# Kernel optimization log

Measured on AMD Instinct MI355X. Metric: run time of the kernel, lower is better.

The kernel has to match this reference:

```python
import jax, jax.numpy as jnp
import numpy as np

B, N, D = 8, 1024, 768
H = 12
HD = D // H
LN_EPS = 1e-5
EPS = 1e-8


def setup_inputs() -> dict:
    key = jax.random.key(0)
    ks = jax.random.split(key, 16)
    s = 0.02
    return {
        "x": jax.random.normal(ks[0], (B, N, D), jnp.float32),
        "low_freq_feat": jax.random.normal(ks[1], (B, N, D), jnp.float32),
        "high_freq_feat": jax.random.normal(ks[2], (B, N, D), jnp.float32),
        "W_qkv_id": jax.random.normal(ks[3], (D, 3 * D), jnp.float32) * s,
        "W_qkv_attr": jax.random.normal(ks[4], (D, 3 * D), jnp.float32) * s,
        "W_fg_id": jax.random.normal(ks[5], (D, D), jnp.float32) * s,
        "b_fg_id": jnp.zeros((D,), jnp.float32),
        "W_fg_attr": jax.random.normal(ks[6], (D, D), jnp.float32) * s,
        "b_fg_attr": jnp.zeros((D,), jnp.float32),
        "W_proj_id": jax.random.normal(ks[7], (D, D), jnp.float32) * s,
        "b_proj_id": jnp.zeros((D,), jnp.float32),
        "W_proj_attr": jax.random.normal(ks[8], (D, D), jnp.float32) * s,
        "b_proj_attr": jnp.zeros((D,), jnp.float32),
        "ln_id_g": jnp.ones((D,), jnp.float32),
        "ln_id_b": jnp.zeros((D,), jnp.float32),
        "ln_attr_g": jnp.ones((D,), jnp.float32),
        "ln_attr_b": jnp.zeros((D,), jnp.float32),
        "ortho_temperature": jnp.float32(1.0),
        "freq_guide_strength": jnp.float32(0.3),
    }


def _layernorm(x, g, b):
    mu = x.mean(-1, keepdims=True)
    var = ((x - mu) ** 2).mean(-1, keepdims=True)
    return (x - mu) * jax.lax.rsqrt(var + LN_EPS) * g + b


def reference(x, low_freq_feat, high_freq_feat,
              W_qkv_id, W_qkv_attr,
              W_fg_id, b_fg_id, W_fg_attr, b_fg_attr,
              W_proj_id, b_proj_id, W_proj_attr, b_proj_attr,
              ln_id_g, ln_id_b, ln_attr_g, ln_attr_b,
              ortho_temperature, freq_guide_strength):
    b, n, d = x.shape
    scale = HD ** -0.5

    def split_qkv(t):
        t = t.reshape(b, n, 3, H, HD).transpose(2, 0, 3, 1, 4)
        return t[0], t[1], t[2]

    q_id, k_id, v_id = split_qkv(x @ W_qkv_id)
    q_at, k_at, v_at = split_qkv(x @ W_qkv_attr)

    fs = jax.nn.sigmoid(freq_guide_strength)
    low_g = (low_freq_feat @ W_fg_id + b_fg_id).reshape(b, n, H, HD).transpose(0, 2, 1, 3)
    high_g = (high_freq_feat @ W_fg_attr + b_fg_attr).reshape(b, n, H, HD).transpose(0, 2, 1, 3)
    v_id = v_id + fs * low_g
    v_at = v_at + fs * high_g

    def soft_attn(q, k):
        a = jnp.clip(jnp.einsum('bhnd,bhmd->bhnm', q, k) * scale, -20.0, 20.0)
        return jax.nn.softmax(a, axis=-1)

    attn_id = soft_attn(q_id, k_id)
    attn_at = soft_attn(q_at, k_at)

    # soft orthogonal mask (same mask for both branches)
    overlap = ((attn_id + EPS) * (attn_at + EPS)).sum(-1, keepdims=True)
    temp = jnp.clip(ortho_temperature, 0.1, 5.0)
    mask = jax.nn.sigmoid(-overlap * temp)

    def mask_renorm(a):
        m = a * mask
        m = m / (m.sum(-1, keepdims=True) + EPS)
        return jnp.where(jnp.isnan(m), jnp.zeros_like(m), m)

    attn_id = mask_renorm(attn_id)
    attn_at = mask_renorm(attn_at)

    def branch_out(a, v, W, bias, g, beta):
        o = jnp.einsum('bhnm,bhmd->bhnd', a, v).transpose(0, 2, 1, 3).reshape(b, n, d)
        return _layernorm(o @ W + bias, g, beta)

    id_features = branch_out(attn_id, v_id, W_proj_id, b_proj_id, ln_id_g, ln_id_b)
    attr_features = branch_out(attn_at, v_at, W_proj_attr, b_proj_attr, ln_attr_g, ln_attr_b)
    return (id_features, attr_features)
```

## Files before the change

kernel.cpp:

```cpp
#include <hip/hip_runtime.h>
#include <stdint.h>


typedef __attribute__((ext_vector_type(8))) _Float16 f16x8;
typedef __attribute__((ext_vector_type(4))) _Float16 f16x4;
typedef __attribute__((ext_vector_type(4))) float    f32x4;

__device__ __forceinline__ void g2l16(const void* g, void* l) {
  __builtin_amdgcn_global_load_lds(
      (const __attribute__((address_space(1))) void*)g,
      (__attribute__((address_space(3))) void*)l, 16, 0, 0);
}

__device__ __forceinline__ void gemm128(const _Float16* __restrict__ A,
                                        const _Float16* __restrict__ Bt,
                                        int K, int m0, int n0,
                                        _Float16* As, _Float16* Bs, f32x4* acc) {
  const int tid = threadIdx.x;
  const int lane = tid & 63, w = tid >> 6;
  const int wm = (w >> 1) * 64, wn = (w & 1) * 64;
  const int l15 = lane & 15, quad = lane >> 4;
  const int srow = lane >> 2;
  const int sg = (lane & 3) ^ ((lane >> 3) & 3);
  const int scol = sg * 8;
  const int rg = (quad ^ ((l15 >> 1) & 3)) * 8;

#pragma unroll
  for (int i = 0; i < 16; i++) acc[i] = (f32x4){0.f, 0.f, 0.f, 0.f};

  const int KB = K >> 5;
#pragma unroll
  for (int i = 0; i < 2; i++) {
    int c = w * 2 + i, row = c * 16 + srow;
    g2l16(A  + (size_t)(m0 + row) * K + scol, As + c * 512);
    g2l16(Bt + (size_t)(n0 + row) * K + scol, Bs + c * 512);
  }
  for (int kb = 0; kb < KB; kb++) {
    __syncthreads();
    f16x8 a[4], b[4];
#pragma unroll
    for (int mt = 0; mt < 4; mt++)
      a[mt] = *(const f16x8*)(As + (wm + mt * 16 + l15) * 32 + rg);
#pragma unroll
    for (int nt = 0; nt < 4; nt++)
      b[nt] = *(const f16x8*)(Bs + (wn + nt * 16 + l15) * 32 + rg);
#pragma unroll
    for (int mt = 0; mt < 4; mt++)
#pragma unroll
      for (int nt = 0; nt < 4; nt++)
        acc[mt * 4 + nt] = __builtin_amdgcn_mfma_f32_16x16x32_f16(
            a[mt], b[nt], acc[mt * 4 + nt], 0, 0, 0);
    __syncthreads();
    if (kb + 1 < KB) {
      int k0 = (kb + 1) * 32;
#pragma unroll
      for (int i = 0; i < 2; i++) {
        int c = w * 2 + i, row = c * 16 + srow;
        g2l16(A  + (size_t)(m0 + row) * K + k0 + scol, As + c * 512);
        g2l16(Bt + (size_t)(n0 + row) * K + k0 + scol, Bs + c * 512);
      }
    }
  }
}

__global__ __launch_bounds__(256) void k_cast3(const float* __restrict__ s0,
                                               const float* __restrict__ s1,
                                               const float* __restrict__ s2,
                                               _Float16* __restrict__ d0,
                                               _Float16* __restrict__ d1,
                                               _Float16* __restrict__ d2) {
  int blk = blockIdx.x;
  const float* s; _Float16* d;
  if (blk < 6144)       { s = s0; d = d0; }
  else if (blk < 12288) { s = s1; d = d1; blk -= 6144; }
  else                  { s = s2; d = d2; blk -= 12288; }
  int i = blk * 256 + threadIdx.x;
  float4 v = ((const float4*)s)[i];
  f16x4 o = {(_Float16)v.x, (_Float16)v.y, (_Float16)v.z, (_Float16)v.w};
  *(f16x4*)(d + (size_t)i * 4) = o;
}

__device__ __forceinline__ void tcast32(const float* __restrict__ src,
                                        _Float16* __restrict__ dst,
                                        int N, int n0, int k0) {
  __shared__ float t[32][33];
  int tr = threadIdx.x >> 5, tc = threadIdx.x & 31;
#pragma unroll
  for (int i = 0; i < 4; i++) {
    int r = tr + i * 8;
    t[r][tc] = src[(size_t)(k0 + r) * N + n0 + tc];
  }
  __syncthreads();
#pragma unroll
  for (int i = 0; i < 4; i++) {
    int r = tr + i * 8;
    dst[(size_t)(n0 + r) * 768 + k0 + tc] = (_Float16)t[tc][r];
  }
}

__global__ __launch_bounds__(256) void k_tcast_qkv(const float* __restrict__ W0,
                                                   const float* __restrict__ W1,
                                                   _Float16* __restrict__ dst) {
  int half = blockIdx.y / 24, yy = blockIdx.y % 24;
  const float* src = half ? W1 : W0;
  _Float16* d = dst + (size_t)half * 2304 * 768;
  tcast32(src, d, 2304, blockIdx.x * 32, yy * 32);
}

__global__ __launch_bounds__(256) void k_tcast4(const float* __restrict__ W0,
                                                const float* __restrict__ W1,
                                                const float* __restrict__ W2,
                                                const float* __restrict__ W3,
                                                _Float16* __restrict__ D0,
                                                _Float16* __restrict__ D1,
                                                _Float16* __restrict__ D2,
                                                _Float16* __restrict__ D3) {
  int q = blockIdx.y / 24, yy = blockIdx.y % 24;
  const float* src; _Float16* d;
  if (q == 0)      { src = W0; d = D0; }
  else if (q == 1) { src = W1; d = D1; }
  else if (q == 2) { src = W2; d = D2; }
  else             { src = W3; d = D3; }
  tcast32(src, d, 768, blockIdx.x * 32, yy * 32);
}

__global__ __launch_bounds__(256) void k_gemm_fg2(const _Float16* __restrict__ Alo,
                                                  const _Float16* __restrict__ Ahi,
                                                  const _Float16* __restrict__ Bid,
                                                  const _Float16* __restrict__ Bat,
                                                  const float* __restrict__ bid,
                                                  const float* __restrict__ bat,
                                                  _Float16* __restrict__ LG,
                                                  _Float16* __restrict__ HG) {
  __shared__ alignas(16) _Float16 As[4096], Bs[4096];
  f32x4 acc[16];
  int half = blockIdx.x / 6;
  int n0 = (blockIdx.x % 6) * 128, m0 = blockIdx.y * 128;
  const _Float16* A = half ? Ahi : Alo;
  const _Float16* Bt = half ? Bat : Bid;
  const float* bias = half ? bat : bid;
  _Float16* out = half ? HG : LG;
  gemm128(A, Bt, 768, m0, n0, As, Bs, acc);
  int lane = threadIdx.x & 63, w = threadIdx.x >> 6;
  int wm = (w >> 1) * 64, wn = (w & 1) * 64, l15 = lane & 15, quad = lane >> 4;
#pragma unroll
  for (int mt = 0; mt < 4; mt++)
#pragma unroll
    for (int nt = 0; nt < 4; nt++) {
      int n = n0 + wn + nt * 16 + l15;
      int m = m0 + wm + mt * 16 + quad * 4;
      float bv = bias[n];
      f32x4 v = acc[mt * 4 + nt];
#pragma unroll
      for (int r = 0; r < 4; r++)
        out[(size_t)(m + r) * 768 + n] = (_Float16)(v[r] + bv);
    }
}

__global__ __launch_bounds__(256) void k_gemm_qkv(const _Float16* __restrict__ A,
                                                  const _Float16* __restrict__ Bt,
                                                  const _Float16* __restrict__ LG,
                                                  const _Float16* __restrict__ HG,
                                                  const float* __restrict__ fgs,
                                                  _Float16* __restrict__ Qb,
                                                  _Float16* __restrict__ Kb,
                                                  _Float16* __restrict__ Vtb) {
  __shared__ alignas(16) _Float16 As[4096], Bs[4096];
  f32x4 acc[16];
  int m0 = blockIdx.y * 128, n0 = blockIdx.x * 128;
  gemm128(A, Bt, 768, m0, n0, As, Bs, acc);
  int lane = threadIdx.x & 63, w = threadIdx.x >> 6;
  int wm = (w >> 1) * 64, wn = (w & 1) * 64, l15 = lane & 15, quad = lane >> 4;
  int br = n0 / 2304;
  int three = (n0 - br * 2304) / 768;
  float fs = 1.f / (1.f + __expf(-fgs[0]));
  float qscl = (three == 0) ? 0.125f * 1.44269504f : 1.0f;
  const _Float16* FG = br ? HG : LG;
#pragma unroll
  for (int mt = 0; mt < 4; mt++)
#pragma unroll
    for (int nt = 0; nt < 4; nt++) {
      int n = n0 + wn + nt * 16 + l15;
      int c = n - br * 2304 - three * 768;
      int h = c >> 6, hd = c & 63;
      int m = m0 + wm + mt * 16 + quad * 4;
      int b = m >> 10, tok = m & 1023;
      size_t head = (size_t)(br * 96 + b * 12 + h);
      f32x4 v = acc[mt * 4 + nt];
      if (three == 2) {
        f16x4 o;
#pragma unroll
        for (int r = 0; r < 4; r++)
          o[r] = (_Float16)(v[r] + fs * (float)FG[(size_t)(m + r) * 768 + c]);
        *(f16x4*)(Vtb + (head * 64 + hd) * 1024 + tok) = o;
      } else {
        _Float16* dst = (three == 0) ? Qb : Kb;
#pragma unroll
        for (int r = 0; r < 4; r++)
          dst[(head * 1024 + tok + r) * 64 + hd] = (_Float16)(v[r] * qscl);
      }
    }
}

__global__ __launch_bounds__(256, 3) void k_attn(const _Float16* __restrict__ Qb,
                                                 const _Float16* __restrict__ Kb,
                                                 const _Float16* __restrict__ Vtb,
                                                 _Float16* __restrict__ Ob) {
  __shared__ alignas(16) _Float16 Qs[128 * 64];
  __shared__ alignas(16) _Float16 Ks[128 * 64];
  __shared__ alignas(16) _Float16 Vts[64 * 128];
  int hl = blockIdx.x;
  int br = hl / 96, bh = hl % 96;
  int qbase = blockIdx.y * 128;
  const _Float16* Qh = Qb + (size_t)hl * 65536;
  const _Float16* Kh = Kb + (size_t)hl * 65536;
  const _Float16* Vth = Vtb + (size_t)hl * 65536;
  int lane = threadIdx.x & 63, w = threadIdx.x >> 6;
  int l15 = lane & 15, quad = lane >> 4;
  const int key7 = l15 & 7;

  {
    int rr = lane >> 3, sg = (lane & 7) ^ rr;
#pragma unroll
    for (int i = 0; i < 4; i++) {
      int c = w * 4 + i;
      g2l16(Qh + (size_t)(qbase + c * 8 + rr) * 64 + sg * 8, Qs + c * 512);
    }
  }
  auto stage_kv = [&](int n0) {
    int rr8 = lane >> 3, sg8 = ((lane & 7) ^ rr8) * 8;
    int rr16 = lane >> 4;
#pragma unroll
    for (int i = 0; i < 4; i++) {
      int c = w * 4 + i;
      g2l16(Kh + (size_t)(n0 + c * 8 + rr8) * 64 + sg8, Ks + c * 512);
      int vrow = c * 4 + rr16;
      int sg16 = ((lane & 15) ^ (vrow & 15)) * 8;
      g2l16(Vth + (size_t)vrow * 1024 + n0 + sg16, Vts + c * 512);
    }
  };
  stage_kv(0);

  f32x4 o[2][4];
#pragma unroll
  for (int qg = 0; qg < 2; qg++)
#pragma unroll
    for (int i = 0; i < 4; i++) o[qg][i] = (f32x4){0.f, 0.f, 0.f, 0.f};
  float rs0 = 0.f, rs1 = 0.f;
  f16x8 bq[2][2];
  const f32x4 zero = (f32x4){0.f, 0.f, 0.f, 0.f};
  const int g0 = (quad ^ key7) * 8, g1 = ((4 + quad) ^ key7) * 8;

  for (int kt = 0; kt < 8; kt++) {
    __syncthreads();
    if (kt == 0) {
#pragma unroll
      for (int qg = 0; qg < 2; qg++) {
        bq[qg][0] = *(const f16x8*)(Qs + (w * 32 + qg * 16 + l15) * 64 + g0);
        bq[qg][1] = *(const f16x8*)(Qs + (w * 32 + qg * 16 + l15) * 64 + g1);
      }
    }
    f32x4 c0, c1;
    {
      f16x8 a0 = *(const f16x8*)(Ks + l15 * 64 + g0);
      f16x8 a1 = *(const f16x8*)(Ks + l15 * 64 + g1);
      c0 = __builtin_amdgcn_mfma_f32_16x16x32_f16(a0, bq[0][0], zero, 0, 0, 0);
      c0 = __builtin_amdgcn_mfma_f32_16x16x32_f16(a1, bq[0][1], c0, 0, 0, 0);
      c1 = __builtin_amdgcn_mfma_f32_16x16x32_f16(a0, bq[1][0], zero, 0, 0, 0);
      c1 = __builtin_amdgcn_mfma_f32_16x16x32_f16(a1, bq[1][1], c1, 0, 0, 0);
    }
#pragma unroll
    for (int nt = 0; nt < 8; nt++) {
      f32x4 n0_, n1_;
      if (nt < 7) {
        f16x8 a0 = *(const f16x8*)(Ks + ((nt + 1) * 16 + l15) * 64 + g0);
        f16x8 a1 = *(const f16x8*)(Ks + ((nt + 1) * 16 + l15) * 64 + g1);
        n0_ = __builtin_amdgcn_mfma_f32_16x16x32_f16(a0, bq[0][0], zero, 0, 0, 0);
        n0_ = __builtin_amdgcn_mfma_f32_16x16x32_f16(a1, bq[0][1], n0_, 0, 0, 0);
        n1_ = __builtin_amdgcn_mfma_f32_16x16x32_f16(a0, bq[1][0], zero, 0, 0, 0);
        n1_ = __builtin_amdgcn_mfma_f32_16x16x32_f16(a1, bq[1][1], n1_, 0, 0, 0);
      }
      f16x4 pt0, pt1;
#pragma unroll
      for (int r = 0; r < 4; r++) {
        float p = __builtin_amdgcn_exp2f(c0[r]);
        rs0 += p; pt0[r] = (_Float16)p;
      }
#pragma unroll
      for (int r = 0; r < 4; r++) {
        float p = __builtin_amdgcn_exp2f(c1[r]);
        rs1 += p; pt1[r] = (_Float16)p;
      }
#pragma unroll
      for (int hdt = 0; hdt < 4; hdt++) {
        int g = ((2 * nt + (quad >> 1)) ^ l15) * 8 + (quad & 1) * 4;
        f16x4 av = *(const f16x4*)(Vts + (hdt * 16 + l15) * 128 + g);
        o[0][hdt] = __builtin_amdgcn_mfma_f32_16x16x16f16(av, pt0, o[0][hdt], 0, 0, 0);
        o[1][hdt] = __builtin_amdgcn_mfma_f32_16x16x16f16(av, pt1, o[1][hdt], 0, 0, 0);
      }
      if (nt < 7) { c0 = n0_; c1 = n1_; }
    }
    __syncthreads();
    if (kt < 7) stage_kv((kt + 1) * 128);
  }
  int b = bh / 12, h = bh % 12;
#pragma unroll
  for (int qg = 0; qg < 2; qg++) {
    float l = qg ? rs1 : rs0;
    l += __shfl_xor(l, 16);
    l += __shfl_xor(l, 32);
    float inv = 1.f / l;
    size_t rowb = ((size_t)br * 8192 + b * 1024 + qbase + w * 32 + qg * 16 + l15) * 768 +
                  h * 64;
#pragma unroll
    for (int hdt = 0; hdt < 4; hdt++) {
      f16x4 u;
#pragma unroll
      for (int r = 0; r < 4; r++) u[r] = (_Float16)(o[qg][hdt][r] * inv);
      *(f16x4*)(Ob + rowb + hdt * 16 + quad * 4) = u;
    }
  }
}

__global__ __launch_bounds__(256) void k_gemm_proj2(const _Float16* __restrict__ Aid,
                                                    const _Float16* __restrict__ Aat,
                                                    const _Float16* __restrict__ Bid,
                                                    const _Float16* __restrict__ Bat,
                                                    float* __restrict__ Yid,
                                                    float* __restrict__ Yat) {
  __shared__ alignas(16) _Float16 As[4096], Bs[4096];
  f32x4 acc[16];
  int half = blockIdx.x / 6;
  int n0 = (blockIdx.x % 6) * 128, m0 = blockIdx.y * 128;
  const _Float16* A = half ? Aat : Aid;
  const _Float16* Bt = half ? Bat : Bid;
  float* Y = half ? Yat : Yid;
  gemm128(A, Bt, 768, m0, n0, As, Bs, acc);
  int lane = threadIdx.x & 63, w = threadIdx.x >> 6;
  int wm = (w >> 1) * 64, wn = (w & 1) * 64, l15 = lane & 15, quad = lane >> 4;
#pragma unroll
  for (int mt = 0; mt < 4; mt++)
#pragma unroll
    for (int nt = 0; nt < 4; nt++) {
      int n = n0 + wn + nt * 16 + l15;
      int m = m0 + wm + mt * 16 + quad * 4;
      f32x4 v = acc[mt * 4 + nt];
#pragma unroll
      for (int r = 0; r < 4; r++) Y[(size_t)(m + r) * 768 + n] = v[r];
    }
}

__global__ __launch_bounds__(256) void k_ln(const float* __restrict__ Yid,
                                            const float* __restrict__ Yat,
                                            const float* __restrict__ bp_id,
                                            const float* __restrict__ bp_at,
                                            const float* __restrict__ g_id,
                                            const float* __restrict__ be_id,
                                            const float* __restrict__ g_at,
                                            const float* __restrict__ be_at,
                                            float* __restrict__ out) {
  int w = threadIdx.x >> 6, lane = threadIdx.x & 63;
  int r = blockIdx.x * 4 + w;
  int br = r >> 13, m = r & 8191;
  const float* Y = br ? Yat : Yid;
  const float* bp = br ? bp_at : bp_id;
  const float* g = br ? g_at : g_id;
  const float* be = br ? be_at : be_id;
  float v[12], sum = 0.f, sq = 0.f;
#pragma unroll
  for (int i = 0; i < 12; i++) {
    int c = lane + i * 64;
    float t = Y[(size_t)m * 768 + c] + bp[c];
    v[i] = t; sum += t; sq += t * t;
  }
#pragma unroll
  for (int d = 1; d < 64; d <<= 1) { sum += __shfl_xor(sum, d); sq += __shfl_xor(sq, d); }
  float mu = sum * (1.f / 768.f);
  float var = sq * (1.f / 768.f) - mu * mu;
  float rstd = rsqrtf(var + 1e-5f);
  float* op = out + (size_t)br * 6291456 + (size_t)m * 768;
#pragma unroll
  for (int i = 0; i < 12; i++) {
    int c = lane + i * 64;
    op[c] = (v[i] - mu) * rstd * g[c] + be[c];
  }
}

extern "C" void kernel_launch(void* const* d_in, const int* in_sizes, int n_in,
                              void* d_out, int out_size, void* d_ws, size_t ws_size,
                              hipStream_t stream) {
  const float* x       = (const float*)d_in[0];
  const float* lowf    = (const float*)d_in[1];
  const float* highf   = (const float*)d_in[2];
  const float* Wqkv_id = (const float*)d_in[3];
  const float* Wqkv_at = (const float*)d_in[4];
  const float* Wfg_id  = (const float*)d_in[5];
  const float* bfg_id  = (const float*)d_in[6];
  const float* Wfg_at  = (const float*)d_in[7];
  const float* bfg_at  = (const float*)d_in[8];
  const float* Wpr_id  = (const float*)d_in[9];
  const float* bpr_id  = (const float*)d_in[10];
  const float* Wpr_at  = (const float*)d_in[11];
  const float* bpr_at  = (const float*)d_in[12];
  const float* g_id    = (const float*)d_in[13];
  const float* be_id   = (const float*)d_in[14];
  const float* g_at    = (const float*)d_in[15];
  const float* be_at   = (const float*)d_in[16];
  const float* fgs     = (const float*)d_in[18];

  char* ws = (char*)d_ws;
  _Float16* x_f    = (_Float16*)(ws + 0);
  _Float16* low_f  = (_Float16*)(ws + 12582912);
  _Float16* high_f = (_Float16*)(ws + 25165824);
  _Float16* wqkvt  = (_Float16*)(ws + 37748736);
  _Float16* wfgidt = (_Float16*)(ws + 44826624);
  _Float16* wfgatt = (_Float16*)(ws + 46006272);
  _Float16* wpridt = (_Float16*)(ws + 47185920);
  _Float16* wpratt = (_Float16*)(ws + 48365568);
  _Float16* LG     = (_Float16*)(ws + 49545216);
  _Float16* HG     = (_Float16*)(ws + 62128128);
  _Float16* Qb     = (_Float16*)(ws + 74711040);
  _Float16* Kb     = (_Float16*)(ws + 99876864);
  _Float16* Vtb    = (_Float16*)(ws + 125042688);
  _Float16* Ob     = (_Float16*)(ws + 150208512);
  float* Y_id = (float*)(ws + 0);
  float* Y_at = (float*)(ws + 49545216);

  k_cast3<<<18432, 256, 0, stream>>>(x, lowf, highf, x_f, low_f, high_f);
  k_tcast_qkv<<<dim3(72, 48), 256, 0, stream>>>(Wqkv_id, Wqkv_at, wqkvt);
  k_tcast4<<<dim3(24, 96), 256, 0, stream>>>(Wfg_id, Wfg_at, Wpr_id, Wpr_at,
                                             wfgidt, wfgatt, wpridt, wpratt);
  k_gemm_fg2<<<dim3(12, 64), 256, 0, stream>>>(low_f, high_f, wfgidt, wfgatt,
                                               bfg_id, bfg_at, LG, HG);
  k_gemm_qkv<<<dim3(36, 64), 256, 0, stream>>>(x_f, wqkvt, LG, HG, fgs, Qb, Kb, Vtb);
  k_attn<<<dim3(192, 8), 256, 0, stream>>>(Qb, Kb, Vtb, Ob);
  k_gemm_proj2<<<dim3(12, 64), 256, 0, stream>>>(Ob, Ob + 6291456, wpridt, wpratt,
                                                 Y_id, Y_at);
  k_ln<<<4096, 256, 0, stream>>>(Y_id, Y_at, bpr_id, bpr_at, g_id, be_id, g_at, be_at,
                                 (float*)d_out);
}
```

Measured before the change: 425.0 us.

## Fuse freq-guide GEMM into V accumulation, swap MFMA operands for vector stores

Reorders the pipeline so the QKV GEMM writes V first and the freq-guide GEMM then adds fs*(acc+bias) straight into the transposed V buffer. This removes the LG/HG intermediate tensors and their strided reads. A templated operand swap in the MFMA lets Q/K and projection epilogues emit contiguous f16x4 stores instead of scattered scalar writes. Projection output is now stored as fp16 and the LayerNorm kernel is vectorized, halving that intermediate traffic but adding a rounding step before the bias and LayerNorm.

```diff
diff --git a/kernel.cpp b/kernel.cpp
--- a/kernel.cpp
+++ b/kernel.cpp
@@ -12,6 +12,7 @@
       (__attribute__((address_space(3))) void*)l, 16, 0, 0);
 }
 
+template <bool SWAP>
 __device__ __forceinline__ void gemm128(const _Float16* __restrict__ A,
                                         const _Float16* __restrict__ Bt,
                                         int K, int m0, int n0,
@@ -48,8 +49,9 @@
     for (int mt = 0; mt < 4; mt++)
 #pragma unroll
       for (int nt = 0; nt < 4; nt++)
-        acc[mt * 4 + nt] = __builtin_amdgcn_mfma_f32_16x16x32_f16(
-            a[mt], b[nt], acc[mt * 4 + nt], 0, 0, 0);
+        acc[mt * 4 + nt] = SWAP
+            ? __builtin_amdgcn_mfma_f32_16x16x32_f16(b[nt], a[mt], acc[mt * 4 + nt], 0, 0, 0)
+            : __builtin_amdgcn_mfma_f32_16x16x32_f16(a[mt], b[nt], acc[mt * 4 + nt], 0, 0, 0);
     __syncthreads();
     if (kb + 1 < KB) {
       int k0 = (kb + 1) * 32;
@@ -124,81 +126,97 @@
   tcast32(src, d, 768, blockIdx.x * 32, yy * 32);
 }
 
-__global__ __launch_bounds__(256) void k_gemm_fg2(const _Float16* __restrict__ Alo,
-                                                  const _Float16* __restrict__ Ahi,
-                                                  const _Float16* __restrict__ Bid,
-                                                  const _Float16* __restrict__ Bat,
-                                                  const float* __restrict__ bid,
-                                                  const float* __restrict__ bat,
-                                                  _Float16* __restrict__ LG,
-                                                  _Float16* __restrict__ HG) {
-  __shared__ alignas(16) _Float16 As[4096], Bs[4096];
-  f32x4 acc[16];
-  int half = blockIdx.x / 6;
-  int n0 = (blockIdx.x % 6) * 128, m0 = blockIdx.y * 128;
-  const _Float16* A = half ? Ahi : Alo;
-  const _Float16* Bt = half ? Bat : Bid;
-  const float* bias = half ? bat : bid;
-  _Float16* out = half ? HG : LG;
-  gemm128(A, Bt, 768, m0, n0, As, Bs, acc);
-  int lane = threadIdx.x & 63, w = threadIdx.x >> 6;
-  int wm = (w >> 1) * 64, wn = (w & 1) * 64, l15 = lane & 15, quad = lane >> 4;
-#pragma unroll
-  for (int mt = 0; mt < 4; mt++)
-#pragma unroll
-    for (int nt = 0; nt < 4; nt++) {
-      int n = n0 + wn + nt * 16 + l15;
-      int m = m0 + wm + mt * 16 + quad * 4;
-      float bv = bias[n];
-      f32x4 v = acc[mt * 4 + nt];
-#pragma unroll
-      for (int r = 0; r < 4; r++)
-        out[(size_t)(m + r) * 768 + n] = (_Float16)(v[r] + bv);
-    }
-}
-
 __global__ __launch_bounds__(256) void k_gemm_qkv(const _Float16* __restrict__ A,
                                                   const _Float16* __restrict__ Bt,
-                                                  const _Float16* __restrict__ LG,
-                                                  const _Float16* __restrict__ HG,
-                                                  const float* __restrict__ fgs,
                                                   _Float16* __restrict__ Qb,
                                                   _Float16* __restrict__ Kb,
                                                   _Float16* __restrict__ Vtb) {
   __shared__ alignas(16) _Float16 As[4096], Bs[4096];
   f32x4 acc[16];
   int m0 = blockIdx.y * 128, n0 = blockIdx.x * 128;
-  gemm128(A, Bt, 768, m0, n0, As, Bs, acc);
+  int br = n0 / 2304;
+  int three = (n0 - br * 2304) / 768;
   int lane = threadIdx.x & 63, w = threadIdx.x >> 6;
   int wm = (w >> 1) * 64, wn = (w & 1) * 64, l15 = lane & 15, quad = lane >> 4;
-  int br = n0 / 2304;
-  int three = (n0 - br * 2304) / 768;
+
+  if (three == 2) {
+    gemm128<false>(A, Bt, 768, m0, n0, As, Bs, acc);
+#pragma unroll
+    for (int mt = 0; mt < 4; mt++)
+#pragma unroll
+      for (int nt = 0; nt < 4; nt++) {
+        int n = n0 + wn + nt * 16 + l15;
+        int c = n - br * 2304 - 1536;
+        int h = c >> 6, hd = c & 63;
+        int m = m0 + wm + mt * 16 + quad * 4;
+        int b = m >> 10, tok = m & 1023;
+        size_t head = (size_t)(br * 96 + b * 12 + h);
+        f32x4 v = acc[mt * 4 + nt];
+        f16x4 o;
+#pragma unroll
+        for (int r = 0; r < 4; r++) o[r] = (_Float16)v[r];
+        *(f16x4*)(Vtb + (head * 64 + hd) * 1024 + tok) = o;
+      }
+  } else {
+    gemm128<true>(A, Bt, 768, m0, n0, As, Bs, acc);
+    float qscl = (three == 0) ? 0.125f * 1.44269504f : 1.0f;
+    _Float16* dst = (three == 0) ? Qb : Kb;
+#pragma unroll
+    for (int mt = 0; mt < 4; mt++)
+#pragma unroll
+      for (int nt = 0; nt < 4; nt++) {
+        int m = m0 + wm + mt * 16 + l15;
+        int n = n0 + wn + nt * 16 + quad * 4;
+        int c = n - br * 2304 - three * 768;
+        int h = c >> 6, hd = c & 63;
+        int b = m >> 10, tok = m & 1023;
+        size_t head = (size_t)(br * 96 + b * 12 + h);
+        f32x4 v = acc[mt * 4 + nt];
+        f16x4 o;
+#pragma unroll
+        for (int r = 0; r < 4; r++) o[r] = (_Float16)(v[r] * qscl);
+        *(f16x4*)(dst + (head * 1024 + tok) * 64 + hd) = o;
+      }
+  }
+}
+
+__global__ __launch_bounds__(256) void k_gemm_fgadd(const _Float16* __restrict__ Alo,
+                                                    const _Float16* __restrict__ Ahi,
+                                                    const _Float16* __restrict__ Bid,
+                                                    const _Float16* __restrict__ Bat,
+                                                    const float* __restrict__ bid,
+                                                    const float* __restrict__ bat,
+                                                    const float* __restrict__ fgs,
+                                                    _Float16* __restrict__ Vtb) {
+  __shared__ alignas(16) _Float16 As[4096], Bs[4096];
+  f32x4 acc[16];
+  int br = blockIdx.x / 6;
+  int n0 = (blockIdx.x % 6) * 128, m0 = blockIdx.y * 128;
+  const _Float16* A = br ? Ahi : Alo;
+  const _Float16* Bt = br ? Bat : Bid;
+  const float* bias = br ? bat : bid;
+  gemm128<false>(A, Bt, 768, m0, n0, As, Bs, acc);
   float fs = 1.f / (1.f + __expf(-fgs[0]));
-  float qscl = (three == 0) ? 0.125f * 1.44269504f : 1.0f;
-  const _Float16* FG = br ? HG : LG;
+  int lane = threadIdx.x & 63, w = threadIdx.x >> 6;
+  int wm = (w >> 1) * 64, wn = (w & 1) * 64, l15 = lane & 15, quad = lane >> 4;
 #pragma unroll
   for (int mt = 0; mt < 4; mt++)
 #pragma unroll
     for (int nt = 0; nt < 4; nt++) {
-      int n = n0 + wn + nt * 16 + l15;
-      int c = n - br * 2304 - three * 768;
+      int c = n0 + wn + nt * 16 + l15;
       int h = c >> 6, hd = c & 63;
       int m = m0 + wm + mt * 16 + quad * 4;
       int b = m >> 10, tok = m & 1023;
       size_t head = (size_t)(br * 96 + b * 12 + h);
+      float bv = bias[c];
       f32x4 v = acc[mt * 4 + nt];
-      if (three == 2) {
-        f16x4 o;
-#pragma unroll
-        for (int r = 0; r < 4; r++)
-          o[r] = (_Float16)(v[r] + fs * (float)FG[(size_t)(m + r) * 768 + c]);
-        *(f16x4*)(Vtb + (head * 64 + hd) * 1024 + tok) = o;
-      } else {
-        _Float16* dst = (three == 0) ? Qb : Kb;
-#pragma unroll
-        for (int r = 0; r < 4; r++)
-          dst[(head * 1024 + tok + r) * 64 + hd] = (_Float16)(v[r] * qscl);
-      }
+      _Float16* p = Vtb + (head * 64 + hd) * 1024 + tok;
+      f16x4 old = *(const f16x4*)p;
+      f16x4 o;
+#pragma unroll
+      for (int r = 0; r < 4; r++)
+        o[r] = (_Float16)((float)old[r] + fs * (v[r] + bv));
+      *(f16x4*)p = o;
     }
 }
 
@@ -326,32 +344,34 @@
                                                     const _Float16* __restrict__ Aat,
                                                     const _Float16* __restrict__ Bid,
                                                     const _Float16* __restrict__ Bat,
-                                                    float* __restrict__ Yid,
-                                                    float* __restrict__ Yat) {
+                                                    _Float16* __restrict__ Yid,
+                                                    _Float16* __restrict__ Yat) {
   __shared__ alignas(16) _Float16 As[4096], Bs[4096];
   f32x4 acc[16];
   int half = blockIdx.x / 6;
   int n0 = (blockIdx.x % 6) * 128, m0 = blockIdx.y * 128;
   const _Float16* A = half ? Aat : Aid;
   const _Float16* Bt = half ? Bat : Bid;
-  float* Y = half ? Yat : Yid;
-  gemm128(A, Bt, 768, m0, n0, As, Bs, acc);
+  _Float16* Y = half ? Yat : Yid;
+  gemm128<true>(A, Bt, 768, m0, n0, As, Bs, acc);
   int lane = threadIdx.x & 63, w = threadIdx.x >> 6;
   int wm = (w >> 1) * 64, wn = (w & 1) * 64, l15 = lane & 15, quad = lane >> 4;
 #pragma unroll
   for (int mt = 0; mt < 4; mt++)
 #pragma unroll
     for (int nt = 0; nt < 4; nt++) {
-      int n = n0 + wn + nt * 16 + l15;
-      int m = m0 + wm + mt * 16 + quad * 4;
+      int m = m0 + wm + mt * 16 + l15;
+      int n = n0 + wn + nt * 16 + quad * 4;
       f32x4 v = acc[mt * 4 + nt];
-#pragma unroll
-      for (int r = 0; r < 4; r++) Y[(size_t)(m + r) * 768 + n] = v[r];
-    }
-}
-
-__global__ __launch_bounds__(256) void k_ln(const float* __restrict__ Yid,
-                                            const float* __restrict__ Yat,
+      f16x4 o;
+#pragma unroll
+      for (int r = 0; r < 4; r++) o[r] = (_Float16)v[r];
+      *(f16x4*)(Y + (size_t)m * 768 + n) = o;
+    }
+}
+
+__global__ __launch_bounds__(256) void k_ln(const _Float16* __restrict__ Yid,
+                                            const _Float16* __restrict__ Yat,
                                             const float* __restrict__ bp_id,
                                             const float* __restrict__ bp_at,
                                             const float* __restrict__ g_id,
@@ -362,16 +382,21 @@
   int w = threadIdx.x >> 6, lane = threadIdx.x & 63;
   int r = blockIdx.x * 4 + w;
   int br = r >> 13, m = r & 8191;
-  const float* Y = br ? Yat : Yid;
+  const _Float16* Y = br ? Yat : Yid;
   const float* bp = br ? bp_at : bp_id;
   const float* g = br ? g_at : g_id;
   const float* be = br ? be_at : be_id;
   float v[12], sum = 0.f, sq = 0.f;
 #pragma unroll
-  for (int i = 0; i < 12; i++) {
-    int c = lane + i * 64;
-    float t = Y[(size_t)m * 768 + c] + bp[c];
-    v[i] = t; sum += t; sq += t * t;
+  for (int j = 0; j < 3; j++) {
+    int c = j * 256 + lane * 4;
+    f16x4 y = *(const f16x4*)(Y + (size_t)m * 768 + c);
+    float4 bv = *(const float4*)(bp + c);
+#pragma unroll
+    for (int r2 = 0; r2 < 4; r2++) {
+      float t = (float)y[r2] + ((const float*)&bv)[r2];
+      v[j * 4 + r2] = t; sum += t; sq += t * t;
+    }
   }
 #pragma unroll
   for (int d = 1; d < 64; d <<= 1) { sum += __shfl_xor(sum, d); sq += __shfl_xor(sq, d); }
@@ -380,9 +405,16 @@
   float rstd = rsqrtf(var + 1e-5f);
   float* op = out + (size_t)br * 6291456 + (size_t)m * 768;
 #pragma unroll
-  for (int i = 0; i < 12; i++) {
-    int c = lane + i * 64;
-    op[c] = (v[i] - mu) * rstd * g[c] + be[c];
+  for (int j = 0; j < 3; j++) {
+    int c = j * 256 + lane * 4;
+    float4 gv = *(const float4*)(g + c);
+    float4 bev = *(const float4*)(be + c);
+    float4 ov;
+#pragma unroll
+    for (int r2 = 0; r2 < 4; r2++)
+      ((float*)&ov)[r2] = (v[j * 4 + r2] - mu) * rstd * ((const float*)&gv)[r2] +
+                          ((const float*)&bev)[r2];
+    *(float4*)(op + c) = ov;
   }
 }
 
@@ -417,22 +449,20 @@
   _Float16* wfgatt = (_Float16*)(ws + 46006272);
   _Float16* wpridt = (_Float16*)(ws + 47185920);
   _Float16* wpratt = (_Float16*)(ws + 48365568);
-  _Float16* LG     = (_Float16*)(ws + 49545216);
-  _Float16* HG     = (_Float16*)(ws + 62128128);
   _Float16* Qb     = (_Float16*)(ws + 74711040);
   _Float16* Kb     = (_Float16*)(ws + 99876864);
   _Float16* Vtb    = (_Float16*)(ws + 125042688);
   _Float16* Ob     = (_Float16*)(ws + 150208512);
-  float* Y_id = (float*)(ws + 0);
-  float* Y_at = (float*)(ws + 49545216);
+  _Float16* Y_id   = (_Float16*)(ws + 0);
+  _Float16* Y_at   = (_Float16*)(ws + 49545216);
 
   k_cast3<<<18432, 256, 0, stream>>>(x, lowf, highf, x_f, low_f, high_f);
   k_tcast_qkv<<<dim3(72, 48), 256, 0, stream>>>(Wqkv_id, Wqkv_at, wqkvt);
   k_tcast4<<<dim3(24, 96), 256, 0, stream>>>(Wfg_id, Wfg_at, Wpr_id, Wpr_at,
                                              wfgidt, wfgatt, wpridt, wpratt);
-  k_gemm_fg2<<<dim3(12, 64), 256, 0, stream>>>(low_f, high_f, wfgidt, wfgatt,
-                                               bfg_id, bfg_at, LG, HG);
-  k_gemm_qkv<<<dim3(36, 64), 256, 0, stream>>>(x_f, wqkvt, LG, HG, fgs, Qb, Kb, Vtb);
+  k_gemm_qkv<<<dim3(36, 64), 256, 0, stream>>>(x_f, wqkvt, Qb, Kb, Vtb);
+  k_gemm_fgadd<<<dim3(12, 64), 256, 0, stream>>>(low_f, high_f, wfgidt, wfgatt,
+                                                 bfg_id, bfg_at, fgs, Vtb);
   k_attn<<<dim3(192, 8), 256, 0, stream>>>(Qb, Kb, Vtb, Ob);
   k_gemm_proj2<<<dim3(12, 64), 256, 0, stream>>>(Ob, Ob + 6291456, wpridt, wpratt,
                                                  Y_id, Y_at);
```

Result: no change. 419.3 us (-1.4%).
